# Performance work log

Hardware: AMD Instinct MI355X
Metric: run time of the kernel (lower is better)

## Reference

```python
import jax, jax.numpy as jnp
import numpy as np

N_NODES = 100000
EPS = 1e-5


def _layernorm(x, gamma, beta):
    mu = jnp.mean(x, axis=-1, keepdims=True)
    var = jnp.mean(jnp.square(x - mu), axis=-1, keepdims=True)
    return (x - mu) * jax.lax.rsqrt(var + EPS) * gamma + beta


def _gcn_layer(src, dst, feat, gamma, beta, W, b):
    # copy_u + sum: aggregate source features into destination nodes
    agg = jax.ops.segment_sum(feat[src], dst, num_segments=N_NODES)
    h = _layernorm(agg, gamma, beta)
    return h @ W + b


def setup_inputs() -> dict:
    key = jax.random.key(0)
    ks = jax.random.split(key, 16)
    d_in, d_hid, d_out = 128, 128, 128
    E = 1600000

    def lin(k, fan_in, fan_out):
        kw, kb = jax.random.split(k)
        lim = 1.0 / np.sqrt(fan_in)
        W = jax.random.uniform(kw, (fan_in, fan_out), jnp.float32, -lim, lim)
        b = jax.random.uniform(kb, (fan_out,), jnp.float32, -lim, lim)
        return W, b

    W1, b1 = lin(ks[0], d_in, d_hid)
    W2, b2 = lin(ks[1], d_hid, d_hid)
    W3, b3 = lin(ks[2], d_hid, d_out)
    return {
        "features": jax.random.normal(ks[3], (N_NODES, d_in), jnp.float32),
        "src": jax.random.randint(ks[4], (E,), 0, N_NODES, jnp.int32),
        "dst": jax.random.randint(ks[5], (E,), 0, N_NODES, jnp.int32),
        "g1": jnp.ones((d_in,), jnp.float32), "be1": jnp.zeros((d_in,), jnp.float32),
        "W1": W1, "b1": b1,
        "g2": jnp.ones((d_hid,), jnp.float32), "be2": jnp.zeros((d_hid,), jnp.float32),
        "W2": W2, "b2": b2,
        "g3": jnp.ones((d_hid,), jnp.float32), "be3": jnp.zeros((d_hid,), jnp.float32),
        "W3": W3, "b3": b3,
    }


def reference(features, src, dst, g1, be1, W1, b1, g2, be2, W2, b2, g3, be3, W3, b3):
    x = jax.nn.relu(_gcn_layer(src, dst, features, g1, be1, W1, b1))
    x = jax.nn.relu(_gcn_layer(src, dst, x, g2, be2, W2, b2))
    x = _gcn_layer(src, dst, x, g3, be3, W3, b3)
    return x
```

## Files before the change

kernel.cpp:

```cpp
#include <hip/hip_runtime.h>
#include <hip/hip_bf16.h>
#include <stdint.h>

typedef unsigned short u16;
typedef __attribute__((ext_vector_type(8))) short short8;
typedef __attribute__((ext_vector_type(4))) float f32x4;

#define DIM 128
#define CAP 64
#define LROW 68

__device__ __forceinline__ float bflo(uint32_t v) {
    uint32_t b = v << 16;
    float f; __builtin_memcpy(&f, &b, 4); return f;
}
__device__ __forceinline__ float bfhi(uint32_t v) {
    uint32_t b = v & 0xffff0000u;
    float f; __builtin_memcpy(&f, &b, 4); return f;
}
__device__ __forceinline__ u16 f2bf(float f) {
    uint32_t x; __builtin_memcpy(&x, &f, 4);
    uint32_t r = (x + 0x7fffu + ((x >> 16) & 1u)) >> 16;
    return (u16)r;
}
__device__ __forceinline__ uint32_t pack2bf(float a, float b) {
    return (uint32_t)f2bf(a) | ((uint32_t)f2bf(b) << 16);
}


__global__ __launch_bounds__(256) void k_bin1(
    const int* __restrict__ src, const int* __restrict__ dst,
    uint32_t* __restrict__ gCur, uint32_t* __restrict__ groupBuf,
    int E, int ngrp, int gcap)
{
    __shared__ uint32_t hcnt[512];
    __shared__ uint32_t hbase[512];
    __shared__ uint32_t hcur[512];
    int nb = gridDim.x;
    int per = (E + nb - 1) / nb;
    int lo = blockIdx.x * per;
    int hi = lo + per; if (hi > E) hi = E;

    for (int t = threadIdx.x; t < ngrp; t += 256) { hcnt[t] = 0; hcur[t] = 0; }
    __syncthreads();

    for (int i = lo + threadIdx.x; i < hi; i += 256)
        atomicAdd(&hcnt[((uint32_t)dst[i]) >> 8], 1u);
    __syncthreads();

    int rot = (blockIdx.x * 37) % (ngrp > 0 ? ngrp : 1);
    for (int k = threadIdx.x; k < ngrp; k += 256) {
        int t = k + rot; if (t >= ngrp) t -= ngrp;
        uint32_t c = hcnt[t];
        hbase[t] = c ? atomicAdd(&gCur[t], c) : 0u;
    }
    __syncthreads();

    for (int i = lo + threadIdx.x; i < hi; i += 256) {
        uint32_t d = (uint32_t)dst[i];
        uint32_t g = d >> 8;
        uint32_t off = hbase[g] + atomicAdd(&hcur[g], 1u);
        if (off < (uint32_t)gcap)
            groupBuf[(size_t)g * gcap + off] = (uint32_t)src[i] | ((d & 255u) << 20);
    }
}

__global__ __launch_bounds__(256) void k_bin2(
    const uint32_t* __restrict__ groupBuf, const uint32_t* __restrict__ gCur,
    uint32_t* __restrict__ bucket, uint32_t* __restrict__ cnt,
    int N, int gcap)
{
    __shared__ uint32_t ncur[256];
    int g = blockIdx.x;
    ncur[threadIdx.x] = 0;
    __syncthreads();
    uint32_t m = gCur[g]; if (m > (uint32_t)gcap) m = gcap;
    int nodebase = g << 8;
    const uint32_t* buf = groupBuf + (size_t)g * gcap;
    for (uint32_t i = threadIdx.x; i < m; i += 256) {
        uint32_t v = buf[i];
        uint32_t nl = v >> 20;
        uint32_t s = v & 0xFFFFFu;
        uint32_t pos = atomicAdd(&ncur[nl], 1u);
        if (pos < CAP) bucket[(size_t)(nodebase + (int)nl) * CAP + pos] = s;
    }
    __syncthreads();
    int node = nodebase + threadIdx.x;
    if (node < N) cnt[node] = ncur[threadIdx.x];
}


__global__ void k_prep(const float* __restrict__ feat, uint32_t* __restrict__ X0,
                       uint32_t* __restrict__ X1, uint32_t* __restrict__ X2, int N,
                       const float* __restrict__ W1, const float* __restrict__ W2,
                       const float* __restrict__ W3,
                       u16* __restrict__ t0, u16* __restrict__ t1, u16* __restrict__ t2)
{
    int b = blockIdx.x;
    if (b < 3) {
        const float* w = b == 0 ? W1 : (b == 1 ? W2 : W3);
        u16* o = b == 0 ? t0 : (b == 1 ? t1 : t2);
        for (int idx = threadIdx.x; idx < DIM * DIM; idx += blockDim.x) {
            int r = idx >> 7, c = idx & 127;
            o[c * DIM + r] = f2bf(w[idx]);
        }
    } else if (b == 3) {
        int t = threadIdx.x;
        if (t < 64)       X0[(size_t)N * 64 + t] = 0u;
        else if (t < 128) X1[(size_t)N * 64 + (t - 64)] = 0u;
        else if (t < 192) X2[(size_t)N * 64 + (t - 128)] = 0u;
    } else {
        int n4 = N * 32;
        int i = (b - 4) * 256 + threadIdx.x;
        int stride = (gridDim.x - 4) * 256;
        const float4* in4 = (const float4*)feat;
        uint2* out2 = (uint2*)X0;
        for (; i < n4; i += stride) {
            float4 v = in4[i];
            uint2 r;
            r.x = pack2bf(v.x, v.y);
            r.y = pack2bf(v.z, v.w);
            out2[i] = r;
        }
    }
}


template <int RELU, int OUTF32>
__global__ __launch_bounds__(512) void k_fused(
    const uint32_t* __restrict__ xin, const uint32_t* __restrict__ cnt,
    const uint32_t* __restrict__ bucket,
    const int* __restrict__ src, const int* __restrict__ dst,
    const float* __restrict__ gamma, const float* __restrict__ beta,
    const u16* __restrict__ wt, const float* __restrict__ bias,
    void* __restrict__ outp, int N, int E)
{
    __shared__ uint32_t lds[16 * LROW];
    int w = threadIdx.x >> 6, l = threadIdx.x & 63;
    int base = blockIdx.x * 16;

    int node0 = __builtin_amdgcn_readfirstlane(base + 2 * w);
    int node1 = node0 + 1;
    int n0c = node0 < N ? node0 : N - 1;
    int n1c = node1 < N ? node1 : N - 1;
    uint32_t c0 = (node0 < N) ? cnt[n0c] : 0u;
    uint32_t c1 = (node1 < N) ? cnt[n1c] : 0u;
    float a0 = 0.f, a1 = 0.f, b0 = 0.f, b1 = 0.f;

    if (__builtin_expect(c0 > CAP || c1 > CAP, 0)) {
        for (int e = 0; e < E; ++e) {
            int d = dst[e];
            if (d == node0) { uint32_t v = xin[(size_t)src[e] * 64 + l]; a0 += bflo(v); a1 += bfhi(v); }
            else if (d == node1) { uint32_t v = xin[(size_t)src[e] * 64 + l]; b0 += bflo(v); b1 += bfhi(v); }
        }
    } else {
        {
            uint32_t bktv = bucket[(size_t)n0c * CAP + l];
#pragma unroll
            for (int g = 0; g < 4; ++g) {
                if ((uint32_t)(g * 16) < c0) {
                    uint32_t v[16];
#pragma unroll
                    for (int i = 0; i < 16; ++i) {
                        const int SLOT = g * 16 + i;
                        uint32_t su = (uint32_t)__builtin_amdgcn_readfirstlane(
                            (int)((uint32_t)__builtin_amdgcn_readlane(bktv, SLOT)));
                        su = ((uint32_t)SLOT < c0) ? su : (uint32_t)N;
                        v[i] = (xin + (size_t)su * 64)[l];
                    }
#pragma unroll
                    for (int i = 0; i < 16; ++i) { a0 += bflo(v[i]); a1 += bfhi(v[i]); }
                }
            }
        }
        {
            uint32_t bktv = bucket[(size_t)n1c * CAP + l];
#pragma unroll
            for (int g = 0; g < 4; ++g) {
                if ((uint32_t)(g * 16) < c1) {
                    uint32_t v[16];
#pragma unroll
                    for (int i = 0; i < 16; ++i) {
                        const int SLOT = g * 16 + i;
                        uint32_t su = (uint32_t)__builtin_amdgcn_readfirstlane(
                            (int)((uint32_t)__builtin_amdgcn_readlane(bktv, SLOT)));
                        su = ((uint32_t)SLOT < c1) ? su : (uint32_t)N;
                        v[i] = (xin + (size_t)su * 64)[l];
                    }
#pragma unroll
                    for (int i = 0; i < 16; ++i) { b0 += bflo(v[i]); b1 += bfhi(v[i]); }
                }
            }
        }
    }

    float sA = a0 + a1, qA = a0 * a0 + a1 * a1;
    float sB = b0 + b1, qB = b0 * b0 + b1 * b1;
    for (int off = 32; off; off >>= 1) {
        sA += __shfl_xor(sA, off, 64);
        sB += __shfl_xor(sB, off, 64);
        qA += __shfl_xor(qA, off, 64);
        qB += __shfl_xor(qB, off, 64);
    }
    float gg0 = gamma[2 * l], gg1 = gamma[2 * l + 1];
    float bb0 = beta[2 * l],  bb1 = beta[2 * l + 1];
    {
        float mean = sA * (1.f / 128.f);
        float var  = qA * (1.f / 128.f) - mean * mean;
        float rs   = rsqrtf(var + 1e-5f);
        lds[(2 * w) * LROW + l] =
            pack2bf((a0 - mean) * rs * gg0 + bb0, (a1 - mean) * rs * gg1 + bb1);
    }
    {
        float mean = sB * (1.f / 128.f);
        float var  = qB * (1.f / 128.f) - mean * mean;
        float rs   = rsqrtf(var + 1e-5f);
        lds[(2 * w + 1) * LROW + l] =
            pack2bf((b0 - mean) * rs * gg0 + bb0, (b1 - mean) * rs * gg1 + bb1);
    }
    __syncthreads();

    int lr = l & 15, lg = l >> 4;
    const u16* ldsu = (const u16*)lds;

    short8 afrag[4];
#pragma unroll
    for (int kc = 0; kc < 4; ++kc)
        afrag[kc] = *(const short8*)&ldsu[lr * (LROW * 2) + kc * 32 + lg * 8];

    int col = w * 16 + lr;
    short8 bfrag[4];
#pragma unroll
    for (int kc = 0; kc < 4; ++kc)
        bfrag[kc] = *(const short8*)(wt + (size_t)col * DIM + kc * 32 + lg * 8);

    f32x4 acc = {0.f, 0.f, 0.f, 0.f};
#pragma unroll
    for (int kc = 0; kc < 4; ++kc)
        acc = __builtin_amdgcn_mfma_f32_16x16x32_bf16(afrag[kc], bfrag[kc], acc, 0, 0, 0);

    float bv = bias[col];
#pragma unroll
    for (int j = 0; j < 4; ++j) {
        int row = base + lg * 4 + j;
        float v = acc[j] + bv;
        if (RELU) v = fmaxf(v, 0.f);
        if (row < N) {
            if (OUTF32) ((float*)outp)[(size_t)row * DIM + col] = v;
            else        ((u16*)outp)[(size_t)row * DIM + col] = f2bf(v);
        }
    }
}


extern "C" void kernel_launch(void* const* d_in, const int* in_sizes, int n_in,
                              void* d_out, int out_size, void* d_ws, size_t ws_size,
                              hipStream_t stream) {
    const float* feat = (const float*)d_in[0];
    const int* src  = (const int*)d_in[1];
    const int* dst  = (const int*)d_in[2];
    const float* g1 = (const float*)d_in[3],  *be1 = (const float*)d_in[4];
    const float* W1 = (const float*)d_in[5],  *b1  = (const float*)d_in[6];
    const float* g2 = (const float*)d_in[7],  *be2 = (const float*)d_in[8];
    const float* W2 = (const float*)d_in[9],  *b2  = (const float*)d_in[10];
    const float* g3 = (const float*)d_in[11], *be3 = (const float*)d_in[12];
    const float* W3 = (const float*)d_in[13], *b3  = (const float*)d_in[14];

    int N = in_sizes[0] / DIM;
    int E = in_sizes[1];
    float* out = (float*)d_out;

    int ngrp = (N + 255) >> 8;
    int gcap = (E / (ngrp > 0 ? ngrp : 1)) * 3 / 2 + 1024;

    char* ws = (char*)d_ws;
    auto alloc = [&](size_t bytes) {
        char* p = ws;
        ws += (bytes + 255) & ~(size_t)255;
        return p;
    };
    uint32_t* gCur     = (uint32_t*)alloc((size_t)ngrp * 4);
    uint32_t* groupBuf = (uint32_t*)alloc((size_t)ngrp * gcap * 4);
    uint32_t* cnt      = (uint32_t*)alloc((size_t)N * 4);
    uint32_t* bucket   = (uint32_t*)alloc((size_t)N * CAP * 4);
    u16* wt1 = (u16*)alloc(DIM * DIM * 2);
    u16* wt2 = (u16*)alloc(DIM * DIM * 2);
    u16* wt3 = (u16*)alloc(DIM * DIM * 2);
    uint32_t* X0 = (uint32_t*)alloc((size_t)(N + 1) * 64 * 4);
    uint32_t* X1 = (uint32_t*)alloc((size_t)(N + 1) * 64 * 4);
    uint32_t* X2 = (uint32_t*)alloc((size_t)(N + 1) * 64 * 4);

    hipMemsetAsync(gCur, 0, (size_t)ngrp * 4, stream);
    k_bin1<<<512, 256, 0, stream>>>(src, dst, gCur, groupBuf, E, ngrp, gcap);
    k_bin2<<<ngrp, 256, 0, stream>>>(groupBuf, gCur, bucket, cnt, N, gcap);
    k_prep<<<1028, 256, 0, stream>>>(feat, X0, X1, X2, N, W1, W2, W3, wt1, wt2, wt3);

    int fblocks = (N + 15) / 16;

    k_fused<1, 0><<<fblocks, 512, 0, stream>>>(X0, cnt, bucket, src, dst, g1, be1, wt1, b1, X1,  N, E);
    k_fused<1, 0><<<fblocks, 512, 0, stream>>>(X1, cnt, bucket, src, dst, g2, be2, wt2, b2, X2,  N, E);
    k_fused<0, 1><<<fblocks, 512, 0, stream>>>(X2, cnt, bucket, src, dst, g3, be3, wt3, b3, out, N, E);
}
```

Baseline: 291.4 us.

## Merge edge binning with feature prep kernel, widen bin2, hoist weight loads

```diff
diff --git a/kernel.cpp b/kernel.cpp
--- a/kernel.cpp
+++ b/kernel.cpp
@@ -8,7 +8,8 @@
 
 #define DIM 128
 #define CAP 64
-#define LROW 68
+#define LROW 69
+#define NB1 512
 
 __device__ __forceinline__ float bflo(uint32_t v) {
     uint32_t b = v << 16;
@@ -28,91 +29,64 @@
 }
 
 
-__global__ __launch_bounds__(256) void k_bin1(
+__global__ __launch_bounds__(256) void k_build(
     const int* __restrict__ src, const int* __restrict__ dst,
     uint32_t* __restrict__ gCur, uint32_t* __restrict__ groupBuf,
-    int E, int ngrp, int gcap)
-{
-    __shared__ uint32_t hcnt[512];
-    __shared__ uint32_t hbase[512];
-    __shared__ uint32_t hcur[512];
-    int nb = gridDim.x;
-    int per = (E + nb - 1) / nb;
-    int lo = blockIdx.x * per;
-    int hi = lo + per; if (hi > E) hi = E;
-
-    for (int t = threadIdx.x; t < ngrp; t += 256) { hcnt[t] = 0; hcur[t] = 0; }
-    __syncthreads();
-
-    for (int i = lo + threadIdx.x; i < hi; i += 256)
-        atomicAdd(&hcnt[((uint32_t)dst[i]) >> 8], 1u);
-    __syncthreads();
-
-    int rot = (blockIdx.x * 37) % (ngrp > 0 ? ngrp : 1);
-    for (int k = threadIdx.x; k < ngrp; k += 256) {
-        int t = k + rot; if (t >= ngrp) t -= ngrp;
-        uint32_t c = hcnt[t];
-        hbase[t] = c ? atomicAdd(&gCur[t], c) : 0u;
-    }
-    __syncthreads();
-
-    for (int i = lo + threadIdx.x; i < hi; i += 256) {
-        uint32_t d = (uint32_t)dst[i];
-        uint32_t g = d >> 8;
-        uint32_t off = hbase[g] + atomicAdd(&hcur[g], 1u);
-        if (off < (uint32_t)gcap)
-            groupBuf[(size_t)g * gcap + off] = (uint32_t)src[i] | ((d & 255u) << 20);
-    }
-}
-
-__global__ __launch_bounds__(256) void k_bin2(
-    const uint32_t* __restrict__ groupBuf, const uint32_t* __restrict__ gCur,
-    uint32_t* __restrict__ bucket, uint32_t* __restrict__ cnt,
-    int N, int gcap)
-{
-    __shared__ uint32_t ncur[256];
-    int g = blockIdx.x;
-    ncur[threadIdx.x] = 0;
-    __syncthreads();
-    uint32_t m = gCur[g]; if (m > (uint32_t)gcap) m = gcap;
-    int nodebase = g << 8;
-    const uint32_t* buf = groupBuf + (size_t)g * gcap;
-    for (uint32_t i = threadIdx.x; i < m; i += 256) {
-        uint32_t v = buf[i];
-        uint32_t nl = v >> 20;
-        uint32_t s = v & 0xFFFFFu;
-        uint32_t pos = atomicAdd(&ncur[nl], 1u);
-        if (pos < CAP) bucket[(size_t)(nodebase + (int)nl) * CAP + pos] = s;
-    }
-    __syncthreads();
-    int node = nodebase + threadIdx.x;
-    if (node < N) cnt[node] = ncur[threadIdx.x];
-}
-
-
-__global__ void k_prep(const float* __restrict__ feat, uint32_t* __restrict__ X0,
-                       uint32_t* __restrict__ X1, uint32_t* __restrict__ X2, int N,
-                       const float* __restrict__ W1, const float* __restrict__ W2,
-                       const float* __restrict__ W3,
-                       u16* __restrict__ t0, u16* __restrict__ t1, u16* __restrict__ t2)
+    int E, int ngrp, int gcap,
+    const float* __restrict__ feat, uint32_t* __restrict__ X0,
+    uint32_t* __restrict__ X1, uint32_t* __restrict__ X2, int N,
+    const float* __restrict__ W1, const float* __restrict__ W2,
+    const float* __restrict__ W3,
+    u16* __restrict__ t0, u16* __restrict__ t1, u16* __restrict__ t2)
 {
     int b = blockIdx.x;
-    if (b < 3) {
-        const float* w = b == 0 ? W1 : (b == 1 ? W2 : W3);
-        u16* o = b == 0 ? t0 : (b == 1 ? t1 : t2);
+    if (b < NB1) {
+        __shared__ uint32_t hcnt[512];
+        __shared__ uint32_t hbase[512];
+        __shared__ uint32_t hcur[512];
+        int per = (E + NB1 - 1) / NB1;
+        int lo = b * per;
+        int hi = lo + per; if (hi > E) hi = E;
+
+        for (int t = threadIdx.x; t < ngrp; t += 256) { hcnt[t] = 0; hcur[t] = 0; }
+        __syncthreads();
+
+        for (int i = lo + threadIdx.x; i < hi; i += 256)
+            atomicAdd(&hcnt[((uint32_t)dst[i]) >> 8], 1u);
+        __syncthreads();
+
+        int rot = (b * 37) % (ngrp > 0 ? ngrp : 1);
+        for (int k = threadIdx.x; k < ngrp; k += 256) {
+            int t = k + rot; if (t >= ngrp) t -= ngrp;
+            uint32_t c = hcnt[t];
+            hbase[t] = c ? atomicAdd(&gCur[t], c) : 0u;
+        }
+        __syncthreads();
+
+        for (int i = lo + threadIdx.x; i < hi; i += 256) {
+            uint32_t d = (uint32_t)dst[i];
+            uint32_t g = d >> 8;
+            uint32_t off = hbase[g] + atomicAdd(&hcur[g], 1u);
+            if (off < (uint32_t)gcap)
+                groupBuf[(size_t)g * gcap + off] = (uint32_t)src[i] | ((d & 255u) << 20);
+        }
+    } else if (b < NB1 + 3) {
+        int wi = b - NB1;
+        const float* w = wi == 0 ? W1 : (wi == 1 ? W2 : W3);
+        u16* o = wi == 0 ? t0 : (wi == 1 ? t1 : t2);
         for (int idx = threadIdx.x; idx < DIM * DIM; idx += blockDim.x) {
             int r = idx >> 7, c = idx & 127;
             o[c * DIM + r] = f2bf(w[idx]);
         }
-    } else if (b == 3) {
+    } else if (b == NB1 + 3) {
         int t = threadIdx.x;
         if (t < 64)       X0[(size_t)N * 64 + t] = 0u;
         else if (t < 128) X1[(size_t)N * 64 + (t - 64)] = 0u;
         else if (t < 192) X2[(size_t)N * 64 + (t - 128)] = 0u;
     } else {
         int n4 = N * 32;
-        int i = (b - 4) * 256 + threadIdx.x;
-        int stride = (gridDim.x - 4) * 256;
+        int i = (b - (NB1 + 4)) * 256 + threadIdx.x;
+        int stride = (gridDim.x - (NB1 + 4)) * 256;
         const float4* in4 = (const float4*)feat;
         uint2* out2 = (uint2*)X0;
         for (; i < n4; i += stride) {
@@ -123,6 +97,31 @@
             out2[i] = r;
         }
     }
+}
+
+
+__global__ __launch_bounds__(512) void k_bin2(
+    const uint32_t* __restrict__ groupBuf, const uint32_t* __restrict__ gCur,
+    uint32_t* __restrict__ bucket, uint32_t* __restrict__ cnt,
+    int N, int gcap)
+{
+    __shared__ uint32_t ncur[256];
+    int g = blockIdx.x;
+    if (threadIdx.x < 256) ncur[threadIdx.x] = 0;
+    __syncthreads();
+    uint32_t m = gCur[g]; if (m > (uint32_t)gcap) m = gcap;
+    int nodebase = g << 8;
+    const uint32_t* buf = groupBuf + (size_t)g * gcap;
+    for (uint32_t i = threadIdx.x; i < m; i += 512) {
+        uint32_t v = buf[i];
+        uint32_t nl = v >> 20;
+        uint32_t s = v & 0xFFFFFu;
+        uint32_t pos = atomicAdd(&ncur[nl], 1u);
+        if (pos < CAP) bucket[(size_t)(nodebase + (int)nl) * CAP + pos] = s;
+    }
+    __syncthreads();
+    int node = nodebase + threadIdx.x;
+    if (threadIdx.x < 256 && node < N) cnt[node] = ncur[threadIdx.x];
 }
 
 
@@ -138,6 +137,14 @@
     __shared__ uint32_t lds[16 * LROW];
     int w = threadIdx.x >> 6, l = threadIdx.x & 63;
     int base = blockIdx.x * 16;
+    int lr = l & 15, lg = l >> 4;
+
+    int col = w * 16 + lr;
+    short8 bfrag[4];
+#pragma unroll
+    for (int kc = 0; kc < 4; ++kc)
+        bfrag[kc] = *(const short8*)(wt + (size_t)col * DIM + kc * 32 + lg * 8);
+    float bv = bias[col];
 
     int node0 = __builtin_amdgcn_readfirstlane(base + 2 * w);
     int node1 = node0 + 1;
@@ -220,26 +227,17 @@
     }
     __syncthreads();
 
-    int lr = l & 15, lg = l >> 4;
     const u16* ldsu = (const u16*)lds;
-
     short8 afrag[4];
 #pragma unroll
     for (int kc = 0; kc < 4; ++kc)
         afrag[kc] = *(const short8*)&ldsu[lr * (LROW * 2) + kc * 32 + lg * 8];
 
-    int col = w * 16 + lr;
-    short8 bfrag[4];
-#pragma unroll
-    for (int kc = 0; kc < 4; ++kc)
-        bfrag[kc] = *(const short8*)(wt + (size_t)col * DIM + kc * 32 + lg * 8);
-
     f32x4 acc = {0.f, 0.f, 0.f, 0.f};
 #pragma unroll
     for (int kc = 0; kc < 4; ++kc)
         acc = __builtin_amdgcn_mfma_f32_16x16x32_bf16(afrag[kc], bfrag[kc], acc, 0, 0, 0);
 
-    float bv = bias[col];
 #pragma unroll
     for (int j = 0; j < 4; ++j) {
         int row = base + lg * 4 + j;
@@ -291,9 +289,9 @@
     uint32_t* X2 = (uint32_t*)alloc((size_t)(N + 1) * 64 * 4);
 
     hipMemsetAsync(gCur, 0, (size_t)ngrp * 4, stream);
-    k_bin1<<<512, 256, 0, stream>>>(src, dst, gCur, groupBuf, E, ngrp, gcap);
-    k_bin2<<<ngrp, 256, 0, stream>>>(groupBuf, gCur, bucket, cnt, N, gcap);
-    k_prep<<<1028, 256, 0, stream>>>(feat, X0, X1, X2, N, W1, W2, W3, wt1, wt2, wt3);
+    k_build<<<NB1 + 4 + 1024, 256, 0, stream>>>(src, dst, gCur, groupBuf, E, ngrp, gcap,
+                                                feat, X0, X1, X2, N, W1, W2, W3, wt1, wt2, wt3);
+    k_bin2<<<ngrp, 512, 0, stream>>>(groupBuf, gCur, bucket, cnt, N, gcap);
 
     int fblocks = (N + 15) / 16;
 
```

After: 265.1 us. 9.0% less time.
